# Kernel optimization log

Measured on AMD Instinct MI355X. Metric: run time of the kernel, lower is better.

The kernel has to match this reference:

```python
import jax, jax.numpy as jnp
import numpy as np

N_ANCHORS = 9
OUTPUT_STRIDE = 16
TOP_N = 2000
NMS_IOU_THRESH = 0.7
MIN_SIZE = 0.01
EPS = 1e-7  # K.epsilon()


def setup_inputs() -> dict:
    key = jax.random.key(0)
    k1, k2 = jax.random.split(key)
    b, h, w = 8, 64, 64  # 1024px image / stride 16
    scores = jax.random.uniform(k1, (b, h, w, N_ANCHORS), jnp.float32)
    offsets = jax.random.normal(k2, (b, h, w, 4 * N_ANCHORS), jnp.float32) * 0.2
    scales = np.array([128.0, 256.0, 512.0])
    ratios = np.array([0.5, 1.0, 2.0])
    aw = (scales[:, None] * np.sqrt(ratios)[None, :]).reshape(-1)
    ah = (scales[:, None] / np.sqrt(ratios)[None, :]).reshape(-1)
    anchors = jnp.asarray(np.stack([aw, ah], axis=-1), jnp.float32)  # [9,2]
    return {"scores": scores, "offsets": offsets, "anchors": anchors}


def _pairwise_iou(a, b):
    # a: [N,4], b: [M,4] (x1,y1,x2,y2) -> [N,M]
    a = a[:, None, :]
    b = b[None, :, :]
    mins = jnp.maximum(a[..., :2], b[..., :2])
    maxs = jnp.minimum(a[..., 2:], b[..., 2:])
    wh = jnp.maximum(maxs - mins, 0.0)
    inter = wh[..., 0] * wh[..., 1]
    area_a = (a[..., 2] - a[..., 0]) * (a[..., 3] - a[..., 1])
    area_b = (b[..., 2] - b[..., 0]) * (b[..., 3] - b[..., 1])
    return inter / (area_a + area_b - inter + EPS)


def _nms_pad(boxes):
    # boxes: [N,4] already sorted by descending score (output of top_k).
    # Greedy NMS (matches tf.image.non_max_suppression semantics), keep order,
    # zero-pad suppressed tail (matches tf.pad to top_n in the original).
    N = boxes.shape[0]
    iou = _pairwise_iou(boxes, boxes)  # [N,N]
    idx = jnp.arange(N)

    def body(i, keep):
        suppress = keep[i] & (iou[i] > NMS_IOU_THRESH) & (idx > i)
        return keep & ~suppress

    keep = jax.lax.fori_loop(0, N, body, jnp.ones((N,), bool))
    sort_keys = jnp.where(keep, idx, N)          # kept indices first, in score order
    order = jnp.argsort(sort_keys)
    valid = (jnp.sort(sort_keys) < N).astype(boxes.dtype)
    return boxes[order] * valid[:, None]


def reference(scores, offsets, anchors):
    b, h, w, K = scores.shape
    off = offsets.reshape(b, h, w, K, 4)
    # anchor decode
    gx, gy = jnp.meshgrid(jnp.arange(w), jnp.arange(h))          # [h,w] each
    center = (jnp.stack([gx, gy], -1).astype(jnp.float32) + 0.5) * OUTPUT_STRIDE  # [h,w,2]
    center = center[:, :, None, :]                               # [h,w,1,2]
    img_wh = jnp.array([w, h], jnp.float32) * OUTPUT_STRIDE
    anc = anchors.reshape(1, 1, 1, K, 2)
    pred_wh = jnp.exp(off[..., 2:]) * anc / img_wh               # [b,h,w,K,2]
    pred_xcyc = (anc * off[..., :2] + center) / img_wh
    box5 = jnp.concatenate([pred_xcyc - pred_wh / 2.0,
                            pred_xcyc + pred_wh / 2.0,
                            scores[..., None]], axis=-1)         # [b,h,w,K,5]
    # filter: clip to [0,1], zero out tiny boxes
    box5 = jnp.clip(box5, 0.0, 1.0)
    wh = box5[..., 2:4] - box5[..., 0:2]
    valid = ((wh[..., 0] > MIN_SIZE) & (wh[..., 1] > MIN_SIZE)).astype(box5.dtype)
    box5 = box5 * valid[..., None]
    box5 = box5.reshape(b, -1, 5)                                # [b, h*w*K, 5]
    # per-image top-k by score, then NMS, then zero-pad to TOP_N
    _, top_i = jax.lax.top_k(box5[..., 4], TOP_N)                # [b, TOP_N]
    top_boxes = jnp.take_along_axis(box5[..., :4], top_i[..., None], axis=1)
    proposals = jax.vmap(_nms_pad)(top_boxes)                    # [b, TOP_N, 4]
    return proposals
```

## Files before the change

kernel.cpp:

```cpp
#include <hip/hip_runtime.h>
#include <stdint.h>

#pragma clang fp contract(off)

#define BATCH 8
#define HH 64
#define WW 64
#define KA 9
#define NBOX (HH * WW * KA)
#define TOPN 2000
#define NPAD 2048
#define NW 32
#define IOU_T 0.7f
#define MINSZ 0.01f
#define EPSF 1e-7f
#define TSTRIDE 33
#define CANDCAP 3072

typedef unsigned int u32;
typedef unsigned long long u64;

__device__ __forceinline__ float clamp01(float x) { return fminf(fmaxf(x, 0.0f), 1.0f); }

__device__ __forceinline__ void bar_lds()
{
    asm volatile("s_waitcnt lgkmcnt(0)" ::: "memory");
    __builtin_amdgcn_s_barrier();
}

__device__ __forceinline__ void decode_one(
    const float* __restrict__ scores, const float4* __restrict__ offsets,
    const float* __restrict__ anchors, int gid, int t,
    float4* boxOut, u32* keyOut)
{
    int k = t % KA;
    int pos = t / KA;
    int wx = pos & (WW - 1);
    int hy = pos >> 6;
    float s = scores[gid];
    float4 off = offsets[gid];
    float aw = anchors[2 * k], ah = anchors[2 * k + 1];
    float cx = ((float)wx + 0.5f) * 16.0f;
    float cy = ((float)hy + 0.5f) * 16.0f;
    float pw = (expf(off.z) * aw) / 1024.0f;
    float ph = (expf(off.w) * ah) / 1024.0f;
    float xc = (aw * off.x + cx) / 1024.0f;
    float yc = (ah * off.y + cy) / 1024.0f;
    float x1 = clamp01(xc - pw * 0.5f);
    float y1 = clamp01(yc - ph * 0.5f);
    float x2 = clamp01(xc + pw * 0.5f);
    float y2 = clamp01(yc + ph * 0.5f);
    float sc = clamp01(s);
    float m = ((x2 - x1) > MINSZ && (y2 - y1) > MINSZ) ? 1.0f : 0.0f;
    *boxOut = make_float4(x1 * m, y1 * m, x2 * m, y2 * m);
    *keyOut = __float_as_uint(sc * m);
}

__global__ __launch_bounds__(256) void zero_kernel(uint4* __restrict__ p, int n)
{
    int g = blockIdx.x * 256 + threadIdx.x;
    if (g < n) p[g] = make_uint4(0, 0, 0, 0);
}

__global__ __launch_bounds__(256) void decode_kernel(
    const float* __restrict__ scores, const float4* __restrict__ offsets,
    const float* __restrict__ anchors, u32* __restrict__ keys,
    u32* __restrict__ ghist)
{
    __shared__ u32 lhist[4096];
    for (int i = threadIdx.x; i < 4096; i += 256) lhist[i] = 0;
    __syncthreads();

    int gid = blockIdx.x * 256 + threadIdx.x;
    int b = gid / NBOX;
    int t = gid - b * NBOX;
    float4 box; u32 key;
    decode_one(scores, offsets, anchors, gid, t, &box, &key);
    keys[gid] = key;
    atomicAdd(&lhist[key >> 20], 1u);
    __syncthreads();

    for (int i = threadIdx.x; i < 4096; i += 256) {
        u32 v = lhist[i];
        if (v) atomicAdd(&ghist[(b << 12) + i], v);
    }
}

__device__ __forceinline__ void rank_find_4096(
    const u32* __restrict__ histL, u32* __restrict__ partial,
    int r, u32* Bsh, int* Rsh, int tid)
{
    partial[tid] = histL[4 * tid] + histL[4 * tid + 1]
                 + histL[4 * tid + 2] + histL[4 * tid + 3];
    __syncthreads();
    if (tid < 64) {
        int lane = tid;
        u32 s = 0;
#pragma unroll
        for (int q = 0; q < 16; ++q) s += partial[lane * 16 + q];
        u32 suf = s;
#pragma unroll
        for (int d = 1; d < 64; d <<= 1) {
            u32 t = __shfl_down(suf, d);
            if (lane + d < 64) suf += t;
        }
        u32 nxt = __shfl_down(suf, 1);
        if (lane == 63) nxt = 0;
        bool cross = (suf >= (u32)r) && (nxt < (u32)r);
        u64 bal = __ballot(cross);
        int L = (int)(__ffsll((unsigned long long)bal) - 1);
        u32 above = __shfl(nxt, L);
        u32 hv = histL[64 * L + lane];
        u32 suf2 = hv;
#pragma unroll
        for (int d = 1; d < 64; d <<= 1) {
            u32 t = __shfl_down(suf2, d);
            if (lane + d < 64) suf2 += t;
        }
        u32 nxt2 = __shfl_down(suf2, 1);
        if (lane == 63) nxt2 = 0;
        u32 mine2 = suf2 + above;
        nxt2 += above;
        if (mine2 >= (u32)r && nxt2 < (u32)r) {
            *Bsh = (u32)(64 * L + lane);
            *Rsh = r - (int)nxt2;
        }
    }
    __syncthreads();
}

__global__ __launch_bounds__(1024) void select_kernel(
    const u32* __restrict__ keys, const u32* __restrict__ ghist,
    const float* __restrict__ scores, const float4* __restrict__ offsets,
    const float* __restrict__ anchors, float4* __restrict__ topBoxes)
{
    int b = blockIdx.x;
    int tid = threadIdx.x;
    int lane = tid & 63;
    const u32* kb = keys + (size_t)b * NBOX;

    __shared__ u32 hist[4096];
    __shared__ u32 partial[1024];
    __shared__ u64 sel[NPAD];
    __shared__ u64 cand[CANDCAP];
    __shared__ u32 Bsh;
    __shared__ int Rsh;
    __shared__ int ctr, cctr;

    if (tid == 0) { ctr = 0; cctr = 0; }
    for (int i = tid; i < 4096; i += 1024) hist[i] = ghist[(b << 12) + i];
    for (int i = tid; i < NPAD; i += 1024) sel[i] = 0ull;
    __syncthreads();
    rank_find_4096(hist, partial, TOPN, &Bsh, &Rsh, tid);
    u32 P1 = Bsh;
    int r1 = Rsh;
    __syncthreads();

    const uint4* kb4 = (const uint4*)kb;
#pragma unroll 1
    for (int it = 0; it < NBOX / 4096; ++it) {
        int i4 = it * 1024 + tid;
        uint4 kv = kb4[i4];
        u32 karr[4] = { kv.x, kv.y, kv.z, kv.w };
        u64 bd[4], bc[4];
        int totd = 0, totc = 0;
#pragma unroll
        for (int q = 0; q < 4; ++q) {
            u32 top = karr[q] >> 20;
            bd[q] = __ballot(top > P1);
            bc[q] = __ballot(top == P1);
            totd += (int)__popcll(bd[q]);
            totc += (int)__popcll(bc[q]);
        }
        int based = 0, basec = 0;
        if (lane == 0) {
            if (totd) based = atomicAdd(&ctr, totd);
            if (totc) basec = atomicAdd(&cctr, totc);
        }
        based = __shfl(based, 0);
        basec = __shfl(basec, 0);
        u64 lmask = (1ull << lane) - 1ull;
        int offd = 0, offc = 0;
#pragma unroll
        for (int q = 0; q < 4; ++q) {
            u32 key = karr[q];
            int i = i4 * 4 + q;
            u64 K = ((u64)key << 16) | (u64)(0xFFFFu - (u32)i);
            u32 top = key >> 20;
            if (top > P1) {
                int slot = based + offd + (int)__popcll(bd[q] & lmask);
                if (slot < NPAD) sel[slot] = K;
            } else if (top == P1) {
                int cslot = basec + offc + (int)__popcll(bc[q] & lmask);
                if (cslot < CANDCAP) cand[cslot] = K;
            }
            offd += (int)__popcll(bd[q]);
            offc += (int)__popcll(bc[q]);
        }
    }
    __syncthreads();
    int cc = cctr < CANDCAP ? cctr : CANDCAP;

    u64 prefix = (u64)P1;
    int r = r1;
    for (int p = 0; p < 3; ++p) {
        int shift = 24 - 12 * p;
        for (int i = tid; i < 4096; i += 1024) hist[i] = 0;
        __syncthreads();
        for (int c = tid; c < cc; c += 1024) {
            u64 K = cand[c];
            if ((K >> (shift + 12)) == prefix)
                atomicAdd(&hist[(u32)((K >> shift) & 0xFFFull)], 1u);
        }
        __syncthreads();
        rank_find_4096(hist, partial, r, &Bsh, &Rsh, tid);
        prefix = (prefix << 12) | (u64)Bsh;
        r = Rsh;
        __syncthreads();
    }
    u64 T48 = prefix;

    for (int c = tid; c < cc; c += 1024) {
        u64 K = cand[c];
        bool take = (K >= T48);
        u64 bal = __ballot(take);
        int base = 0;
        if (lane == 0 && bal) base = atomicAdd(&ctr, (int)__popcll(bal));
        base = __shfl(base, 0);
        if (take) {
            int slot = base + (int)__popcll(bal & ((1ull << lane) - 1ull));
            if (slot < NPAD) sel[slot] = K;
        }
    }
    __syncthreads();

    for (int k = 2; k <= NPAD; k <<= 1) {
        for (int j = k >> 1; j > 0; j >>= 1) {
#pragma unroll
            for (int n = 0; n < 2; ++n) {
                int i = tid + n * 1024;
                int ixj = i ^ j;
                if (ixj > i) {
                    bool desc = ((i & k) == 0);
                    u64 a = sel[i], c = sel[ixj];
                    if (desc ? (a < c) : (a > c)) { sel[i] = c; sel[ixj] = a; }
                }
            }
            __syncthreads();
        }
    }

    for (int i = tid; i < NPAD; i += 1024) {
        float4 v = make_float4(0, 0, 0, 0);
        if (i < TOPN) {
            u64 K = sel[i];
            int idx = 0xFFFF - (int)(K & 0xFFFFull);
            u32 kdummy;
            decode_one(scores, offsets, anchors, b * NBOX + idx, idx, &v, &kdummy);
        }
        topBoxes[b * NPAD + i] = v;
    }
}

__global__ __launch_bounds__(256) void iou_kernel(
    const float4* __restrict__ topBoxes, u64* __restrict__ sup)
{
    int gid = blockIdx.x * 256 + threadIdx.x;
    int wid = gid >> 6;
    int lane = gid & 63;
    int b = wid / TOPN;
    int r = wid - b * TOPN;

    float4 A = topBoxes[(size_t)b * NPAD + r];
    float areaA = (A.z - A.x) * (A.w - A.y);
    size_t supBase = ((size_t)b * NPAD + r) * NW;

    for (int w = r >> 6; w < NW; ++w) {
        int j = w * 64 + lane;
        float4 Bx = topBoxes[(size_t)b * NPAD + j];
        float ix1 = fmaxf(A.x, Bx.x);
        float iy1 = fmaxf(A.y, Bx.y);
        float ix2 = fminf(A.z, Bx.z);
        float iy2 = fminf(A.w, Bx.w);
        float iw = fmaxf(ix2 - ix1, 0.0f);
        float ih = fmaxf(iy2 - iy1, 0.0f);
        float inter = iw * ih;
        float areaB = (Bx.z - Bx.x) * (Bx.w - Bx.y);
        float iou = inter / (areaA + areaB - inter + EPSF);
        bool s = (iou > IOU_T) && (j > r) && (j < TOPN);
        u64 m = __ballot(s);
        if (lane == 0) sup[supBase + w] = m;
    }
}

__global__ __launch_bounds__(256) void resolve_kernel(
    const u64* __restrict__ sup, const float4* __restrict__ topBoxes,
    float4* __restrict__ out)
{
    int b = blockIdx.x;
    int tid = threadIdx.x;
    __shared__ u64 tile[2][64 * TSTRIDE];
    __shared__ u64 keep[NW];
    __shared__ u64 nzmap[NW];
    __shared__ int wbase[NW];
    if (tid < NW) keep[tid] = (tid < 31) ? ~0ull : 0xFFFFull;
    const u64* supB = sup + (size_t)b * NPAD * NW;
    unsigned* keep32 = (unsigned*)keep;

    int row = tid >> 2;
    int wcol = (tid & 3) * 8;

    {
        const uint4* src = (const uint4*)(supB + tid * 8);
        uint4 p0 = src[0], p1 = src[1], p2 = src[2], p3 = src[3];
        u64* d = &tile[0][row * TSTRIDE + wcol];
        d[0] = ((u64)p0.y << 32) | p0.x;  d[1] = ((u64)p0.w << 32) | p0.z;
        d[2] = ((u64)p1.y << 32) | p1.x;  d[3] = ((u64)p1.w << 32) | p1.z;
        d[4] = ((u64)p2.y << 32) | p2.x;  d[5] = ((u64)p2.w << 32) | p2.z;
        d[6] = ((u64)p3.y << 32) | p3.x;  d[7] = ((u64)p3.w << 32) | p3.z;
    }
    bar_lds();

    for (int w = 0; w < NW; ++w) {
        int buf = w & 1;
        uint4 n0, n1, n2, n3;
        if (w + 1 < NW) {
            const uint4* src = (const uint4*)(supB + (size_t)(w + 1) * 2048 + tid * 8);
            n0 = src[0]; n1 = src[1]; n2 = src[2]; n3 = src[3];
        }

        if (tid < 64) {
            u64 m = tile[buf][tid * TSTRIDE + w];
            u64 later = 0;
            for (int w2 = w + 1; w2 < NW; ++w2) later |= tile[buf][tid * TSTRIDE + w2];
            u64 nzAny = __ballot((m | later) != 0ull);
            u64 nzDiag = __ballot(m != 0ull);
            u32 mlo = (u32)m, mhi = (u32)(m >> 32);
            u64 kw64 = keep[w];
            u32 kwlo = (u32)__builtin_amdgcn_readfirstlane((int)(u32)kw64);
            u32 kwhi = (u32)__builtin_amdgcn_readfirstlane((int)(u32)(kw64 >> 32));
            u64 kw = ((u64)kwhi << 32) | kwlo;
            u64 rem = kw & nzDiag;
            while (rem) {
                int t2 = (int)(__ffsll((unsigned long long)rem) - 1);
                u32 alo = (u32)__builtin_amdgcn_readlane((int)mlo, t2);
                u32 ahi = (u32)__builtin_amdgcn_readlane((int)mhi, t2);
                u64 mt = ((u64)ahi << 32) | alo;
                kw &= ~mt;
                rem &= ~(mt | (1ull << t2));
            }
            if (tid == 0) { keep[w] = kw; nzmap[w] = nzAny; }
        }
        bar_lds();

        u64 gate = keep[w] & nzmap[w];
        int w2 = tid & 31;
        int grp = tid >> 5;
        if (w2 > w && gate) {
            u64 acc = 0;
#pragma unroll
            for (int q = 0; q < 8; ++q) {
                int rl = grp * 8 + q;
                if ((gate >> rl) & 1ull)
                    acc |= tile[buf][rl * TSTRIDE + w2];
            }
            if (acc) {
                u32 lo = (u32)acc, hi = (u32)(acc >> 32);
                if (lo) atomicAnd(&keep32[2 * w2], ~lo);
                if (hi) atomicAnd(&keep32[2 * w2 + 1], ~hi);
            }
        }

        if (w + 1 < NW) {
            u64* d = &tile[buf ^ 1][row * TSTRIDE + wcol];
            d[0] = ((u64)n0.y << 32) | n0.x;  d[1] = ((u64)n0.w << 32) | n0.z;
            d[2] = ((u64)n1.y << 32) | n1.x;  d[3] = ((u64)n1.w << 32) | n1.z;
            d[4] = ((u64)n2.y << 32) | n2.x;  d[5] = ((u64)n2.w << 32) | n2.z;
            d[6] = ((u64)n3.y << 32) | n3.x;  d[7] = ((u64)n3.w << 32) | n3.z;
        }
        bar_lds();
    }

    if (tid == 0) {
        int s = 0;
        for (int w2 = 0; w2 < NW; ++w2) { wbase[w2] = s; s += __popcll(keep[w2]); }
    }
    __syncthreads();
    for (int i = tid; i < TOPN; i += 256)
        out[(size_t)b * TOPN + i] = make_float4(0, 0, 0, 0);
    __syncthreads();
    for (int i = tid; i < TOPN; i += 256) {
        int wi = i >> 6, bz = i & 63;
        u64 kw = keep[wi];
        if ((kw >> bz) & 1ull) {
            int pos = wbase[wi] + __popcll(kw & ((1ull << bz) - 1ull));
            out[(size_t)b * TOPN + pos] = topBoxes[(size_t)b * NPAD + i];
        }
    }
}

extern "C" void kernel_launch(void* const* d_in, const int* in_sizes, int n_in,
                              void* d_out, int out_size, void* d_ws, size_t ws_size,
                              hipStream_t stream)
{
    const float*  scores  = (const float*)d_in[0];
    const float4* offsets = (const float4*)d_in[1];
    const float*  anchors = (const float*)d_in[2];
    float4* out = (float4*)d_out;

    char* ws = (char*)d_ws;
    u64*    sup      = (u64*)(ws);
    u32*    keys     = (u32*)(ws + 4194304);
    float4* topBoxes = (float4*)(ws + 5373952);
    u32*    ghist    = (u32*)(ws + 5636096);

    zero_kernel<<<(131072 / 16 + 255) / 256, 256, 0, stream>>>((uint4*)ghist, 131072 / 16);
    decode_kernel<<<(BATCH * NBOX) / 256, 256, 0, stream>>>(scores, offsets, anchors, keys, ghist);
    select_kernel<<<BATCH, 1024, 0, stream>>>(keys, ghist, scores, offsets, anchors, topBoxes);
    iou_kernel<<<(BATCH * TOPN * 64) / 256, 256, 0, stream>>>(topBoxes, sup);
    resolve_kernel<<<BATCH, 256, 0, stream>>>(sup, topBoxes, out);
}
```

Baseline: 116.0 us.

## Run bitonic sort in registers with wavefront shuffles for small strides

The LDS-based bitonic sort of the 2048 selected keys now keeps each thread's two elements in registers. Strides below 64 use __shfl_xor within the wavefront instead of LDS plus a barrier. Stride 1024 compares the two elements a thread already holds, and only strides 64–512 go through LDS exchanges. This cuts most of the __syncthreads barriers and LDS traffic in the sort, at the cost of more register pressure and shuffle instructions.

```diff
diff --git a/kernel.cpp b/kernel.cpp
--- a/kernel.cpp
+++ b/kernel.cpp
@@ -234,31 +234,53 @@
     }
     __syncthreads();
 
+    u64 e0 = sel[tid];
+    u64 e1 = sel[tid + 1024];
+    const int i0 = tid, i1 = tid + 1024;
+
     for (int k = 2; k <= NPAD; k <<= 1) {
-        for (int j = k >> 1; j > 0; j >>= 1) {
-#pragma unroll
-            for (int n = 0; n < 2; ++n) {
-                int i = tid + n * 1024;
-                int ixj = i ^ j;
-                if (ixj > i) {
-                    bool desc = ((i & k) == 0);
-                    u64 a = sel[i], c = sel[ixj];
-                    if (desc ? (a < c) : (a > c)) { sel[i] = c; sel[ixj] = a; }
-                }
+        for (int j = k >> 1; j >= 64; j >>= 1) {
+            if (j == 1024) {
+                u64 mx = e0 > e1 ? e0 : e1;
+                u64 mn = e0 > e1 ? e1 : e0;
+                e0 = mx; e1 = mn;
+            } else {
+                sel[i0] = e0; sel[i1] = e1;
+                __syncthreads();
+                u64 p0 = sel[i0 ^ j];
+                u64 p1 = sel[i1 ^ j];
+                bool kp0 = ((i0 & k) == 0) ^ ((i0 & j) != 0);
+                bool kp1 = ((i1 & k) == 0) ^ ((i1 & j) != 0);
+                e0 = kp0 ? (e0 > p0 ? e0 : p0) : (e0 < p0 ? e0 : p0);
+                e1 = kp1 ? (e1 > p1 ? e1 : p1) : (e1 < p1 ? e1 : p1);
+                __syncthreads();
             }
-            __syncthreads();
-        }
-    }
-
-    for (int i = tid; i < NPAD; i += 1024) {
+        }
+        int jstart = (k >> 1) < 32 ? (k >> 1) : 32;
+        for (int j = jstart; j >= 1; j >>= 1) {
+            u64 p0 = __shfl_xor(e0, j);
+            u64 p1 = __shfl_xor(e1, j);
+            bool kp0 = ((i0 & k) == 0) ^ ((i0 & j) != 0);
+            bool kp1 = ((i1 & k) == 0) ^ ((i1 & j) != 0);
+            e0 = kp0 ? (e0 > p0 ? e0 : p0) : (e0 < p0 ? e0 : p0);
+            e1 = kp1 ? (e1 > p1 ? e1 : p1) : (e1 < p1 ? e1 : p1);
+        }
+    }
+
+    {
+        float4 v; u32 kd;
+        int idx = 0xFFFF - (int)(e0 & 0xFFFFull);
+        decode_one(scores, offsets, anchors, b * NBOX + idx, idx, &v, &kd);
+        topBoxes[b * NPAD + i0] = v;
+    }
+    {
         float4 v = make_float4(0, 0, 0, 0);
-        if (i < TOPN) {
-            u64 K = sel[i];
-            int idx = 0xFFFF - (int)(K & 0xFFFFull);
-            u32 kdummy;
-            decode_one(scores, offsets, anchors, b * NBOX + idx, idx, &v, &kdummy);
-        }
-        topBoxes[b * NPAD + i] = v;
+        if (i1 < TOPN) {
+            u32 kd;
+            int idx = 0xFFFF - (int)(e1 & 0xFFFFull);
+            decode_one(scores, offsets, anchors, b * NBOX + idx, idx, &v, &kd);
+        }
+        topBoxes[b * NPAD + i1] = v;
     }
 }
 
```

Measured after the change: 106.4 us. 1.09x faster.
